# Kernel tuning notes

Hardware: AMD Instinct MI355X
Metric: run time of the kernel (lower is better)

## Reference

```python
import jax, jax.numpy as jnp
import numpy as np

N = 16384      # total ligand atoms
E = 65536      # edges
B = 256        # graphs / batch
MAXN = 64      # atoms per graph (max_nodes for to_dense_batch)
FIN = 64       # num_node_features
HID = 256      # hidden_channels
GH = 2         # gat heads
LP = 1024      # protein length
NH = 4         # cross-attention heads
HD = HID // NH
VOCAB = 22


def setup_inputs() -> dict:
    key = jax.random.key(0)
    ks = jax.random.split(key, 48)
    f = jnp.float32
    def nrm(k, shape, s=0.05):
        return jax.random.normal(k, shape, f) * s
    inp = {}
    inp["x"] = jax.random.normal(ks[0], (N, FIN), f)
    inp["edge_index"] = jax.random.randint(ks[1], (2, E), 0, N)
    inp["batch"] = jnp.arange(N) // MAXN  # sorted, 64 atoms per graph
    inp["protein_seq"] = jax.random.randint(ks[2], (B, LP), 0, VOCAB)
    # GAT layer 1 (FIN -> HID, GH heads, concat=False)
    inp["w1"] = nrm(ks[3], (FIN, GH * HID)); inp["as1"] = nrm(ks[4], (GH, HID)); inp["ad1"] = nrm(ks[5], (GH, HID)); inp["b1"] = jnp.zeros((HID,), f)
    inp["w2"] = nrm(ks[6], (HID, GH * HID)); inp["as2"] = nrm(ks[7], (GH, HID)); inp["ad2"] = nrm(ks[8], (GH, HID)); inp["b2"] = jnp.zeros((HID,), f)
    inp["w3"] = nrm(ks[9], (HID, GH * HID)); inp["as3"] = nrm(ks[10], (GH, HID)); inp["ad3"] = nrm(ks[11], (GH, HID)); inp["b3"] = jnp.zeros((HID,), f)
    # protein embedding + conv1d (OIH layout)
    inp["emb"] = nrm(ks[12], (VOCAB, HID), 0.1)
    inp["conv_w"] = nrm(ks[13], (HID, HID, 3)); inp["conv_b"] = jnp.zeros((HID,), f)
    # cross-attention MHA
    inp["wq"] = nrm(ks[14], (HID, HID)); inp["bq"] = jnp.zeros((HID,), f)
    inp["wk"] = nrm(ks[15], (HID, HID)); inp["bk"] = jnp.zeros((HID,), f)
    inp["wv"] = nrm(ks[16], (HID, HID)); inp["bv"] = jnp.zeros((HID,), f)
    inp["wo"] = nrm(ks[17], (HID, HID)); inp["bo"] = jnp.zeros((HID,), f)
    inp["ln1_g"] = jnp.ones((HID,), f); inp["ln1_b"] = jnp.zeros((HID,), f)
    inp["ffw1"] = nrm(ks[18], (HID, 4 * HID)); inp["ffb1"] = jnp.zeros((4 * HID,), f)
    inp["ffw2"] = nrm(ks[19], (4 * HID, HID)); inp["ffb2"] = jnp.zeros((HID,), f)
    inp["ln2_g"] = jnp.ones((HID,), f); inp["ln2_b"] = jnp.zeros((HID,), f)
    inp["fc1_w"] = nrm(ks[20], (HID, HID)); inp["fc1_b"] = jnp.zeros((HID,), f)
    inp["fc2_w"] = nrm(ks[21], (HID, 1)); inp["fc2_b"] = jnp.zeros((1,), f)
    return inp


def _gat(x, edge_index, W, a_src, a_dst, bias):
    # PyG GATConv, concat=False (mean over heads), add_self_loops=True
    n = x.shape[0]
    h = (x @ W).reshape(n, GH, HID)                      # [N,GH,C]
    loop = jnp.arange(n)
    src = jnp.concatenate([edge_index[0], loop])
    dst = jnp.concatenate([edge_index[1], loop])
    a_s = jnp.einsum('nhc,hc->nh', h, a_src)             # [N,GH]
    a_d = jnp.einsum('nhc,hc->nh', h, a_dst)
    e = jax.nn.leaky_relu(a_s[src] + a_d[dst], 0.2)      # [E+N,GH]
    emax = jax.ops.segment_max(e, dst, num_segments=n)   # each node has a self-loop
    ex = jnp.exp(e - emax[dst])
    den = jax.ops.segment_sum(ex, dst, num_segments=n)
    alpha = ex / den[dst]                                # [E+N,GH]
    msg = h[src] * alpha[:, :, None]
    out = jax.ops.segment_sum(msg, dst, num_segments=n)  # [N,GH,C]
    return out.mean(axis=1) + bias


def _to_dense_batch(x, batch):
    # batch is sorted node->graph ids; counts per graph <= MAXN
    ones = jnp.ones((x.shape[0],), jnp.int32)
    counts = jax.ops.segment_sum(ones, batch, num_segments=B)
    starts = jnp.cumsum(counts) - counts
    pos = jnp.arange(x.shape[0]) - starts[batch]
    dense = jnp.zeros((B, MAXN, x.shape[1]), x.dtype).at[batch, pos].set(x)
    mask = jnp.zeros((B, MAXN), bool).at[batch, pos].set(True)
    return dense, mask


def _layernorm(x, g, b, eps=1e-5):
    mu = x.mean(-1, keepdims=True)
    var = ((x - mu) ** 2).mean(-1, keepdims=True)
    return (x - mu) * jax.lax.rsqrt(var + eps) * g + b


def reference(x, edge_index, batch, protein_seq,
              w1, as1, ad1, b1, w2, as2, ad2, b2, w3, as3, ad3, b3,
              emb, conv_w, conv_b,
              wq, bq, wk, bk, wv, bv, wo, bo,
              ln1_g, ln1_b, ffw1, ffb1, ffw2, ffb2, ln2_g, ln2_b,
              fc1_w, fc1_b, fc2_w, fc2_b):
    # --- ligand GNN (eval mode: dropout = identity) ---
    h = jax.nn.elu(_gat(x, edge_index, w1, as1, ad1, b1))
    h = jax.nn.elu(_gat(h, edge_index, w2, as2, ad2, b2))
    h = jax.nn.elu(_gat(h, edge_index, w3, as3, ad3, b3))
    lig, lig_mask = _to_dense_batch(h, batch)            # [B,MAXN,HID], [B,MAXN]
    # --- protein branch ---
    p = emb[protein_seq]                                 # [B,LP,HID]
    p = p.transpose(0, 2, 1)                             # [B,HID,LP]
    p = jax.lax.conv_general_dilated(p, conv_w, (1,), [(1, 1)],
                                     dimension_numbers=('NCH', 'OIH', 'NCH'))
    p = jax.nn.relu(p + conv_b[None, :, None]).transpose(0, 2, 1)  # [B,LP,HID]
    kpm = protein_seq == 0                               # key padding mask
    # --- cross attention (query=ligand, key/value=protein) ---
    q = (lig @ wq + bq).reshape(B, MAXN, NH, HD)
    k = (p @ wk + bk).reshape(B, LP, NH, HD)
    v = (p @ wv + bv).reshape(B, LP, NH, HD)
    scores = jnp.einsum('bqhd,bkhd->bhqk', q, k) / np.sqrt(HD).astype(np.float32)
    scores = jnp.where(kpm[:, None, None, :], jnp.float32(-1e9), scores)
    attn = jax.nn.softmax(scores, axis=-1)               # [B,NH,MAXN,LP]
    ctx = jnp.einsum('bhqk,bkhd->bqhd', attn, v).reshape(B, MAXN, HID)
    attn_out = ctx @ wo + bo
    y = _layernorm(lig + attn_out, ln1_g, ln1_b)
    ff = jax.nn.gelu(y @ ffw1 + ffb1, approximate=False) @ ffw2 + ffb2
    y = _layernorm(y + ff, ln2_g, ln2_b)
    # --- masked mean pool ---
    m = lig_mask[:, :, None].astype(y.dtype)
    pooled = (y * m).sum(axis=1) / (m.sum(axis=1) + 1e-6)
    out = jax.nn.relu(pooled @ fc1_w + fc1_b)
    return out @ fc2_w + fc2_b                           # [B,1]
```

## Files before the change

kernel.cpp:

```cpp
#include <hip/hip_runtime.h>
#include <hip/hip_bf16.h>
#include <cstdint>
#include <cstddef>

#define NAT 16384
#define NED 65536
#define BGR 256
#define FIN 64
#define HID 256
#define LPN 1024
#define HD 64
#define NTRIP 11638
#define NTAB  11648

typedef __bf16 bf16x8 __attribute__((ext_vector_type(8)));
typedef float floatx4 __attribute__((ext_vector_type(4)));

__device__ __forceinline__ void gl2lds16(const void* g, void* l)
{
    __builtin_amdgcn_global_load_lds(
        (const __attribute__((address_space(1))) unsigned int*)g,
        (__attribute__((address_space(3))) unsigned int*)l, 16, 0, 0);
}

template<int ACT, int OUTBF16, int BIASROW, int HSPLIT, int NCOL>
__global__ __launch_bounds__(512) void gemm_mfma(const __bf16* __restrict__ A,
    const __bf16* __restrict__ Bt, const float* __restrict__ bias,
    void* __restrict__ Cout, int M, int Nn, int K, float escale)
{
    constexpr int NJ = NCOL / 32;
    __shared__ __bf16 As[2][128][32];
    __shared__ __bf16 Bs[2][NCOL][32];
    const int t = threadIdx.x;
    const int m0 = blockIdx.y * 128, n0 = blockIdx.x * NCOL;
    const int w = t >> 6, lane = t & 63;
    const int wm = (w & 3) * 32, wn = (w >> 2) * (NCOL / 2);
    const int quad = lane >> 4, l16 = lane & 15;
    const int r0 = t >> 2, s0 = t & 3, g0 = (s0 ^ (r0 & 3)) * 8;
    const int fso = (quad ^ (l16 & 3)) * 8;
    floatx4 acc[2][NJ] = {};
    for (int k0 = 0; k0 < K; k0 += 64) {
        gl2lds16(A + (size_t)(m0 + r0) * K + k0 + g0,       &As[0][r0][s0 * 8]);
        gl2lds16(A + (size_t)(m0 + r0) * K + k0 + 32 + g0,  &As[1][r0][s0 * 8]);
        if (NCOL == 128 || t < 256) {
            gl2lds16(Bt + (size_t)(n0 + r0) * K + k0 + g0,      &Bs[0][r0][s0 * 8]);
            gl2lds16(Bt + (size_t)(n0 + r0) * K + k0 + 32 + g0, &Bs[1][r0][s0 * 8]);
        }
        __syncthreads();
#pragma unroll
        for (int c = 0; c < 2; c++) {
            bf16x8 af[2], bfr[NJ];
#pragma unroll
            for (int mi = 0; mi < 2; mi++) af[mi]  = *(const bf16x8*)&As[c][wm + mi * 16 + l16][fso];
#pragma unroll
            for (int nj = 0; nj < NJ; nj++) bfr[nj] = *(const bf16x8*)&Bs[c][wn + nj * 16 + l16][fso];
#pragma unroll
            for (int mi = 0; mi < 2; mi++)
#pragma unroll
                for (int nj = 0; nj < NJ; nj++)
                    acc[mi][nj] = __builtin_amdgcn_mfma_f32_16x16x32_bf16(af[mi], bfr[nj], acc[mi][nj], 0, 0, 0);
        }
        __syncthreads();
    }
#pragma unroll
    for (int mi = 0; mi < 2; mi++)
#pragma unroll
        for (int nj = 0; nj < NJ; nj++) {
            int col = n0 + wn + nj * 16 + l16;
#pragma unroll
            for (int r = 0; r < 4; r++) {
                int row = m0 + wm + mi * 16 + quad * 4 + r;
                float bval = bias ? (BIASROW ? bias[row] : bias[col]) : 0.f;
                float v = (acc[mi][nj][r] + bval) * escale;
                if (ACT == 1) v = fmaxf(v, 0.f);
                if (ACT == 2) v = 0.5f * v * (1.f + erff(v * 0.70710678118654752f));
                if (HSPLIT)      ((__bf16*)Cout)[((size_t)(col >> 6) * M + row) * 64 + (col & 63)] = (__bf16)v;
                else if (OUTBF16) ((__bf16*)Cout)[(size_t)row * Nn + col] = (__bf16)v;
                else              ((float*)Cout)[(size_t)row * Nn + col] = v;
            }
        }
}

__global__ __launch_bounds__(512) void gemm_gat(const __bf16* __restrict__ A,
    const __bf16* __restrict__ Bt, const float* __restrict__ as_f,
    const float* __restrict__ ad_f, __bf16* __restrict__ Hg,
    float* __restrict__ part, int K)
{
    __shared__ __bf16 As[2][128][32];
    __shared__ __bf16 Bs[2][128][32];
    const int t = threadIdx.x;
    const int m0 = blockIdx.y * 128, n0 = blockIdx.x * 128;
    const int w = t >> 6, lane = t & 63;
    const int wm = (w & 3) * 32, wn = (w >> 2) * 64;
    const int quad = lane >> 4, l16 = lane & 15;
    const int r0 = t >> 2, s0 = t & 3, g0 = (s0 ^ (r0 & 3)) * 8;
    const int fso = (quad ^ (l16 & 3)) * 8;
    floatx4 acc[2][4] = {};
    for (int k0 = 0; k0 < K; k0 += 64) {
        gl2lds16(A + (size_t)(m0 + r0) * K + k0 + g0,       &As[0][r0][s0 * 8]);
        gl2lds16(A + (size_t)(m0 + r0) * K + k0 + 32 + g0,  &As[1][r0][s0 * 8]);
        gl2lds16(Bt + (size_t)(n0 + r0) * K + k0 + g0,      &Bs[0][r0][s0 * 8]);
        gl2lds16(Bt + (size_t)(n0 + r0) * K + k0 + 32 + g0, &Bs[1][r0][s0 * 8]);
        __syncthreads();
#pragma unroll
        for (int c = 0; c < 2; c++) {
            bf16x8 af[2], bfr[4];
#pragma unroll
            for (int mi = 0; mi < 2; mi++) af[mi]  = *(const bf16x8*)&As[c][wm + mi * 16 + l16][fso];
#pragma unroll
            for (int nj = 0; nj < 4; nj++) bfr[nj] = *(const bf16x8*)&Bs[c][wn + nj * 16 + l16][fso];
#pragma unroll
            for (int mi = 0; mi < 2; mi++)
#pragma unroll
                for (int nj = 0; nj < 4; nj++)
                    acc[mi][nj] = __builtin_amdgcn_mfma_f32_16x16x32_bf16(af[mi], bfr[nj], acc[mi][nj], 0, 0, 0);
        }
        __syncthreads();
    }
    const int slot = blockIdx.x * 2 + (w >> 2);
#pragma unroll
    for (int mi = 0; mi < 2; mi++) {
#pragma unroll
        for (int r = 0; r < 4; r++) {
            float ps = 0.f, pd = 0.f;
#pragma unroll
            for (int nj = 0; nj < 4; nj++) {
                int col = n0 + wn + nj * 16 + l16;
                float v = acc[mi][nj][r];
                ps += v * as_f[col];
                pd += v * ad_f[col];
            }
#pragma unroll
            for (int off = 1; off < 16; off <<= 1) {
                ps += __shfl_xor(ps, off, 64);
                pd += __shfl_xor(pd, off, 64);
            }
            if (l16 == 0) {
                int row = m0 + wm + mi * 16 + quad * 4 + r;
                part[(size_t)(slot * 2 + 0) * NAT + row] = ps;
                part[(size_t)(slot * 2 + 1) * NAT + row] = pd;
            }
        }
    }
#pragma unroll
    for (int mi = 0; mi < 2; mi++)
#pragma unroll
        for (int nj = 0; nj < 4; nj++) {
            int col = n0 + wn + nj * 16 + l16;
#pragma unroll
            for (int r = 0; r < 4; r++) {
                int row = m0 + wm + mi * 16 + quad * 4 + r;
                Hg[(size_t)row * 512 + col] = (__bf16)acc[mi][nj][r];
            }
        }
}

__global__ void fold_k(const float* __restrict__ part, float* __restrict__ a_s,
                       float* __restrict__ a_d)
{
    int n = blockIdx.x * 256 + threadIdx.x;
    float s0 = 0.f, d0 = 0.f, s1 = 0.f, d1 = 0.f;
#pragma unroll
    for (int sl = 0; sl < 4; sl++) {
        s0 += part[(size_t)(sl * 2 + 0) * NAT + n];
        d0 += part[(size_t)(sl * 2 + 1) * NAT + n];
        s1 += part[(size_t)((sl + 4) * 2 + 0) * NAT + n];
        d1 += part[(size_t)((sl + 4) * 2 + 1) * NAT + n];
    }
    a_s[n * 2 + 0] = s0; a_s[n * 2 + 1] = s1;
    a_d[n * 2 + 0] = d0; a_d[n * 2 + 1] = d1;
}

struct Segs {
    const float* src[12];
    __bf16* dst[12];
    int kdim[12];
    int ndim[12];
    int mode[12];
    int start[13];
};

__global__ __launch_bounds__(256) void misc1_k(const int* __restrict__ ei,
    int* __restrict__ deg, const float* __restrict__ emb,
    const float* __restrict__ cw, float* __restrict__ tap,
    const int* __restrict__ seq, unsigned short* __restrict__ tid,
    Segs S, int total)
{
    const int bid = blockIdx.x;
    const int t = threadIdx.x;
    if (bid < 256) {
        int e = bid * 256 + t;
        atomicAdd(&deg[ei[NED + e]], 1);
    } else if (bid < 520) {
        const int b = bid - 256;
        const int dlv = b >> 2, part = b & 3;
        const int dl = dlv / 22, v = dlv % 22;
        const float* er = emb + v * 256 + part * 64;
        const float* wr = cw + (size_t)t * 768 + part * 192 + dl;
        float s = 0.f;
        for (int k = 0; k < 64; k += 4) {
            s += er[k + 0] * wr[k * 3 + 0];
            s += er[k + 1] * wr[k * 3 + 3];
            s += er[k + 2] * wr[k * 3 + 6];
            s += er[k + 3] * wr[k * 3 + 9];
        }
        atomicAdd(&tap[(size_t)dlv * 256 + t], s);
    } else if (bid < 1544) {
        int i = (bid - 520) * 256 + t;
        int b = i >> 10, l = i & 1023;
        const int* sr = seq + b * LPN;
        int t0 = (l > 0) ? sr[l - 1] : -1;
        int t1 = sr[l];
        int t2 = (l < LPN - 1) ? sr[l + 1] : -1;
        int v = (t0 + 1) * 506 + t1 * 23 + (t2 + 1);
        tid[i] = (unsigned short)(v | (t1 == 0 ? 0x8000 : 0));
    } else {
        int i = (bid - 1544) * 256 + t;
        if (i >= total) return;
        int s = 0;
        while (i >= S.start[s + 1]) s++;
        int j = i - S.start[s];
        if (S.mode[s] == 0) {
            S.dst[s][j] = (__bf16)S.src[s][j];
        } else {
            int K = S.kdim[s], N = S.ndim[s];
            int n = j / K, k = j - n * K;
            S.dst[s][j] = (__bf16)S.src[s][(size_t)k * N + n];
        }
    }
}

__global__ __launch_bounds__(256) void misc2_k(const int* __restrict__ deg,
    int* __restrict__ rowptr, const float* __restrict__ tap,
    const float* __restrict__ bias, __bf16* __restrict__ P)
{
    __shared__ int part[256];
    const int t = threadIdx.x;
    if (blockIdx.x == 0) {
        int base = t * 64;
        int s = 0;
#pragma unroll
        for (int i = 0; i < 64; i++) s += deg[base + i];
        part[t] = s;
        __syncthreads();
        for (int off = 1; off < 256; off <<= 1) {
            int v = (t >= off) ? part[t - off] : 0;
            __syncthreads();
            part[t] += v;
            __syncthreads();
        }
        int run = t ? part[t - 1] : 0;
        for (int i = 0; i < 64; i++) { rowptr[base + i] = run; run += deg[base + i]; }
        if (t == 255) rowptr[16384] = run;
    } else {
        const int row = (blockIdx.x - 1) * 8 + (t >> 5);
        const int c = (t & 31) * 8;
        __bf16 o[8];
        if (row < NTRIP) {
            const int a = row / 506, rem = row - a * 506;
            const int t1 = rem / 23, c2 = rem - t1 * 23;
            float acc[8];
#pragma unroll
            for (int j = 0; j < 8; j++) acc[j] = bias[c + j];
            if (a > 0) {
                const float* r = tap + (size_t)(0 * 22 + (a - 1)) * 256 + c;
#pragma unroll
                for (int j = 0; j < 8; j++) acc[j] += r[j];
            }
            {
                const float* r = tap + (size_t)(1 * 22 + t1) * 256 + c;
#pragma unroll
                for (int j = 0; j < 8; j++) acc[j] += r[j];
            }
            if (c2 > 0) {
                const float* r = tap + (size_t)(2 * 22 + (c2 - 1)) * 256 + c;
#pragma unroll
                for (int j = 0; j < 8; j++) acc[j] += r[j];
            }
#pragma unroll
            for (int j = 0; j < 8; j++) o[j] = (__bf16)fmaxf(acc[j], 0.f);
        } else {
#pragma unroll
            for (int j = 0; j < 8; j++) o[j] = (__bf16)0.f;
        }
        *(uint4*)(P + (size_t)row * 256 + c) = *(uint4*)o;
    }
}

__global__ __launch_bounds__(512) void misc3_k(const int* __restrict__ ei,
    int* __restrict__ fill, const int* __restrict__ rowptr,
    int* __restrict__ csrc, int* __restrict__ cdst,
    const __bf16* __restrict__ A, const __bf16* __restrict__ wkT,
    const __bf16* __restrict__ wvT, const float* __restrict__ bk,
    const float* __restrict__ bv, __bf16* __restrict__ Ktab,
    __bf16* __restrict__ Vtab)
{
    __shared__ __bf16 As[2][128][32];
    __shared__ __bf16 Bs[2][128][32];
    const int t = threadIdx.x;
    if (blockIdx.x < 128) {
        int e = blockIdx.x * 512 + t;
        if (e >= NED) return;
        int d = ei[NED + e];
        int pos = rowptr[d] + atomicAdd(&fill[d], 1);
        csrc[pos] = ei[e];
        cdst[pos] = d;
        return;
    }
    const int lb = blockIdx.x - 128;
    const int bx = lb & 3, by = lb >> 2;
    const int z = bx >> 1;
    const int m0 = by * 128, n0 = (bx & 1) * 128;
    const __bf16* Bt = z ? wvT : wkT;
    const float* bias = z ? bv : bk;
    __bf16* Cout = z ? Vtab : Ktab;
    const int w = t >> 6, lane = t & 63;
    const int wm = (w & 3) * 32, wn = (w >> 2) * 64;
    const int quad = lane >> 4, l16 = lane & 15;
    const int r0 = t >> 2, s0 = t & 3, g0 = (s0 ^ (r0 & 3)) * 8;
    const int fso = (quad ^ (l16 & 3)) * 8;
    floatx4 acc[2][4] = {};
    for (int k0 = 0; k0 < 256; k0 += 64) {
        gl2lds16(A + (size_t)(m0 + r0) * 256 + k0 + g0,       &As[0][r0][s0 * 8]);
        gl2lds16(A + (size_t)(m0 + r0) * 256 + k0 + 32 + g0,  &As[1][r0][s0 * 8]);
        gl2lds16(Bt + (size_t)(n0 + r0) * 256 + k0 + g0,      &Bs[0][r0][s0 * 8]);
        gl2lds16(Bt + (size_t)(n0 + r0) * 256 + k0 + 32 + g0, &Bs[1][r0][s0 * 8]);
        __syncthreads();
#pragma unroll
        for (int c = 0; c < 2; c++) {
            bf16x8 af[2], bfr[4];
#pragma unroll
            for (int mi = 0; mi < 2; mi++) af[mi]  = *(const bf16x8*)&As[c][wm + mi * 16 + l16][fso];
#pragma unroll
            for (int nj = 0; nj < 4; nj++) bfr[nj] = *(const bf16x8*)&Bs[c][wn + nj * 16 + l16][fso];
#pragma unroll
            for (int mi = 0; mi < 2; mi++)
#pragma unroll
                for (int nj = 0; nj < 4; nj++)
                    acc[mi][nj] = __builtin_amdgcn_mfma_f32_16x16x32_bf16(af[mi], bfr[nj], acc[mi][nj], 0, 0, 0);
        }
        __syncthreads();
    }
#pragma unroll
    for (int mi = 0; mi < 2; mi++)
#pragma unroll
        for (int nj = 0; nj < 4; nj++) {
            int col = n0 + wn + nj * 16 + l16;
#pragma unroll
            for (int r = 0; r < 4; r++) {
                int row = m0 + wm + mi * 16 + quad * 4 + r;
                float v = acc[mi][nj][r] + bias[col];
                Cout[((size_t)(col >> 6) * NTAB + row) * 64 + (col & 63)] = (__bf16)v;
            }
        }
}

__global__ __launch_bounds__(256) void gat_agg(const int* __restrict__ rowptr,
    const int* __restrict__ csrc, const __bf16* __restrict__ hgb,
    const float* __restrict__ a_s, const float* __restrict__ a_d,
    const float* __restrict__ bias, float* __restrict__ out, __bf16* __restrict__ outb)
{
    const int wave = threadIdx.x >> 6, lane = threadIdx.x & 63;
    const int d = blockIdx.x * 4 + wave;
    const int beg = rowptr[d], end = rowptr[d + 1];
    float2 as2 = *(const float2*)(a_s + d * 2);
    float2 ad2 = *(const float2*)(a_d + d * 2);
    float e0 = as2.x + ad2.x; e0 = (e0 > 0.f) ? e0 : 0.2f * e0;
    float e1 = as2.y + ad2.y; e1 = (e1 > 0.f) ? e1 : 0.2f * e1;
    float m0 = e0, den0 = 1.f, m1 = e1, den1 = 1.f;
    for (int p = beg; p < end; p++) {
        int s = csrc[p];
        float2 av = *(const float2*)(a_s + s * 2);
        float f0 = av.x + ad2.x; f0 = (f0 > 0.f) ? f0 : 0.2f * f0;
        float f1 = av.y + ad2.y; f1 = (f1 > 0.f) ? f1 : 0.2f * f1;
        float nm0 = fmaxf(m0, f0);
        den0 = den0 * __expf(m0 - nm0) + __expf(f0 - nm0);
        m0 = nm0;
        float nm1 = fmaxf(m1, f1);
        den1 = den1 * __expf(m1 - nm1) + __expf(f1 - nm1);
        m1 = nm1;
    }
    const float inv0 = 1.f / den0, inv1 = 1.f / den1;
    const int ch = lane * 8;
    const int g = ch >> 8;
    const float mg = g ? m1 : m0, invg = g ? inv1 : inv0;
    float acc[8] = {};
    {
        float al = __expf((g ? e1 : e0) - mg) * invg;
        bf16x8 hv = *(const bf16x8*)(hgb + (size_t)d * 512 + ch);
#pragma unroll
        for (int j = 0; j < 8; j++) acc[j] += (float)hv[j] * al;
    }
    for (int p = beg; p < end; p++) {
        int s = csrc[p];
        float2 av = *(const float2*)(a_s + s * 2);
        float f0 = av.x + ad2.x; f0 = (f0 > 0.f) ? f0 : 0.2f * f0;
        float f1 = av.y + ad2.y; f1 = (f1 > 0.f) ? f1 : 0.2f * f1;
        float al = __expf((g ? f1 : f0) - mg) * invg;
        bf16x8 hv = *(const bf16x8*)(hgb + (size_t)s * 512 + ch);
#pragma unroll
        for (int j = 0; j < 8; j++) acc[j] += (float)hv[j] * al;
    }
    float other[8];
#pragma unroll
    for (int j = 0; j < 8; j++) other[j] = __shfl_xor(acc[j], 32, 64);
    if (lane < 32) {
#pragma unroll
        for (int j = 0; j < 8; j++) {
            float v = 0.5f * (acc[j] + other[j]) + bias[ch + j];
            v = (v > 0.f) ? v : expm1f(v);
            if (out) out[(size_t)d * 256 + ch + j] = v;
            outb[(size_t)d * 256 + ch + j] = (__bf16)v;
        }
    }
}

__global__ __launch_bounds__(256, 4) void attn6_k(const __bf16* __restrict__ Qb,
    const __bf16* __restrict__ Ktab, const __bf16* __restrict__ Vtab,
    const unsigned short* __restrict__ tid16, __bf16* __restrict__ O)
{
    __shared__ __bf16 Ks[2][4096];
    __shared__ __bf16 Vs[4096];
    __shared__ __bf16 Ps2[4][16][64];
    __shared__ float mask_f[1024];
    __shared__ unsigned short tids[1024];
    const int t = threadIdx.x;
    const int bid = blockIdx.x;
    const int h = (bid >> 1) & 3;
    const int b = ((bid >> 3) << 1) | (bid & 1);
    const int w = t >> 6, lane = t & 63;
    const int quad = lane >> 4, l16 = lane & 15;
    const int key = (l16 & 7) << 4;
    const __bf16* Kh = Ktab + (size_t)h * NTAB * 64;
    const __bf16* Vh = Vtab + (size_t)h * NTAB * 64;
    {
        const uint32_t* src = (const uint32_t*)(tid16 + (size_t)b * LPN);
        uint32_t v0 = src[t], v1 = src[t + 256];
        ((uint32_t*)tids)[t] = v0;
        ((uint32_t*)tids)[t + 256] = v1;
        mask_f[2 * t + 0] = (v0 & 0x8000u) ? -1e9f : 0.f;
        mask_f[2 * t + 1] = (v0 & 0x80000000u) ? -1e9f : 0.f;
        mask_f[2 * (t + 256) + 0] = (v1 & 0x8000u) ? -1e9f : 0.f;
        mask_f[2 * (t + 256) + 1] = (v1 & 0x80000000u) ? -1e9f : 0.f;
    }
    const __bf16* qrow = Qb + (size_t)(b * 64 + w * 16 + l16) * HID + h * HD;
    bf16x8 aq0 = *(const bf16x8*)(qrow + quad * 8);
    bf16x8 aq1 = *(const bf16x8*)(qrow + 32 + quad * 8);
    __syncthreads();

    auto stageK = [&](int kt, int bufb) {
#pragma unroll
        for (int it = 0; it < 2; it++) {
            const int s = it * 256 + t;
            const int pos = s >> 3;
            const int c = (s & 7) ^ (pos & 7);
            const int row = tids[kt * 64 + pos] & 0x7fff;
            gl2lds16(Kh + (size_t)row * 64 + c * 8,
                     &Ks[bufb][(it * 256 + w * 64) * 8]);
        }
    };
    auto loadV = [&](int kt, bf16x8* vrr) {
#pragma unroll
        for (int it = 0; it < 2; it++) {
            const int pos = w * 8 + (lane >> 3) + it * 32;
            const int row = tids[kt * 64 + pos] & 0x7fff;
            vrr[it] = *(const bf16x8*)(Vh + (size_t)row * 64 + (lane & 7) * 8);
        }
    };
    auto writeV = [&](const bf16x8* vrr) {
        const int p = lane >> 3, c = lane & 7;
#pragma unroll
        for (int it = 0; it < 2; it++) {
            const int pos = w * 8 + p + it * 32;
            const int cp = pos >> 3;
#pragma unroll
            for (int j = 0; j < 8; j++) {
                const int chl = c * 8 + j;
                Vs[chl * 64 + (((cp ^ c ^ j) & 7) << 3) + p] = vrr[it][j];
            }
        }
    };

    bf16x8 vr[2];
    stageK(0, 0);
    loadV(0, vr);
    writeV(vr);
    float m_run = -3e38f;
    float l_run = 0.f;
    floatx4 ctx[4] = {};
    __syncthreads();

    for (int kt = 0; kt < 16; kt++) {
        const int buf = kt & 1;
        const int kp0 = kt * 64;
        if (kt < 15) {
            stageK(kt + 1, buf ^ 1);
            loadV(kt + 1, vr);
        }
        const int ksl0 = (quad ^ (l16 & 7)) * 8;
        const int ksl1 = ((quad + 4) ^ (l16 & 7)) * 8;
        floatx4 s[4];
#pragma unroll
        for (int nj = 0; nj < 4; nj++) {
            const __bf16* kr = &Ks[buf][(nj * 16 + l16) * 64];
            bf16x8 k0 = *(const bf16x8*)&kr[ksl0];
            bf16x8 k1 = *(const bf16x8*)&kr[ksl1];
            floatx4 z = {0.f, 0.f, 0.f, 0.f};
            s[nj] = __builtin_amdgcn_mfma_f32_16x16x32_bf16(k0, aq0, z, 0, 0, 0);
            s[nj] = __builtin_amdgcn_mfma_f32_16x16x32_bf16(k1, aq1, s[nj], 0, 0, 0);
        }
#pragma unroll
        for (int nj = 0; nj < 4; nj++) {
            floatx4 m4 = *(const floatx4*)&mask_f[kp0 + nj * 16 + quad * 4];
#pragma unroll
            for (int r = 0; r < 4; r++) s[nj][r] += m4[r];
        }
        float mx = -3e38f;
#pragma unroll
        for (int nj = 0; nj < 4; nj++)
#pragma unroll
            for (int r = 0; r < 4; r++) mx = fmaxf(mx, s[nj][r]);
        mx = fmaxf(mx, __shfl_xor(mx, 16, 64));
        mx = fmaxf(mx, __shfl_xor(mx, 32, 64));
        const float mn = fmaxf(m_run, mx);
        const float alpha = __expf(m_run - mn);
        m_run = mn;
        float rs = 0.f;
#pragma unroll
        for (int nj = 0; nj < 4; nj++)
#pragma unroll
            for (int r = 0; r < 4; r++) {
                float p = __expf(s[nj][r] - mn);
                s[nj][r] = p;
                rs += p;
            }
        rs += __shfl_xor(rs, 16, 64);
        rs += __shfl_xor(rs, 32, 64);
        l_run = l_run * alpha + rs;
        float al[4];
#pragma unroll
        for (int r = 0; r < 4; r++) al[r] = __shfl(alpha, quad * 4 + r, 64);
        {
            char* rowp = (char*)&Ps2[w][l16][0];
#pragma unroll
            for (int nj = 0; nj < 4; nj++) {
                union { uint2 u2; unsigned short us[4]; } pk;
#pragma unroll
                for (int r = 0; r < 4; r++) {
                    __bf16 bv = (__bf16)s[nj][r];
                    pk.us[r] = *(unsigned short*)&bv;
                }
                *(uint2*)(rowp + ((nj * 32 + quad * 8) ^ key)) = pk.u2;
            }
        }
        bf16x8 pa0 = *(const bf16x8*)((char*)&Ps2[w][l16][0] + ((quad * 16) ^ key));
        bf16x8 pa1 = *(const bf16x8*)((char*)&Ps2[w][l16][0] + ((64 + quad * 16) ^ key));
#pragma unroll
        for (int dj = 0; dj < 4; dj++) {
#pragma unroll
            for (int r = 0; r < 4; r++) ctx[dj][r] *= al[r];
            const int chl = dj * 16 + l16;
            const int Xc = ((chl >> 3) ^ (chl & 7)) & 7;
            bf16x8 bv0 = *(const bf16x8*)&Vs[chl * 64 + (((quad ^ Xc) & 7) << 3)];
            bf16x8 bv1 = *(const bf16x8*)&Vs[chl * 64 + ((((quad + 4) ^ Xc) & 7) << 3)];
            ctx[dj] = __builtin_amdgcn_mfma_f32_16x16x32_bf16(pa0, bv0, ctx[dj], 0, 0, 0);
            ctx[dj] = __builtin_amdgcn_mfma_f32_16x16x32_bf16(pa1, bv1, ctx[dj], 0, 0, 0);
        }
        __syncthreads();
        if (kt < 15) writeV(vr);
        __syncthreads();
    }
    float ll[4];
#pragma unroll
    for (int r = 0; r < 4; r++) ll[r] = __shfl(l_run, quad * 4 + r, 64);
#pragma unroll
    for (int dj = 0; dj < 4; dj++)
#pragma unroll
        for (int r = 0; r < 4; r++) {
            int q = w * 16 + quad * 4 + r;
            O[((size_t)(b * 64 + q)) * 256 + h * HD + dj * 16 + l16] = (__bf16)(ctx[dj][r] / ll[r]);
        }
}

__device__ __forceinline__ float blockSum256(float v, float* red)
{
#pragma unroll
    for (int off = 32; off >= 1; off >>= 1) v += __shfl_down(v, off, 64);
    int wave = threadIdx.x >> 6, lane = threadIdx.x & 63;
    if (lane == 0) red[wave] = v;
    __syncthreads();
    float s = red[0] + red[1] + red[2] + red[3];
    __syncthreads();
    return s;
}

__global__ __launch_bounds__(256) void lnres_k(const float* __restrict__ A,
    const float* __restrict__ Bb, const float* __restrict__ g,
    const float* __restrict__ be, float* __restrict__ Y, __bf16* __restrict__ Yb)
{
    __shared__ float red[4];
    int r = blockIdx.x, t = threadIdx.x;
    float v = A[(size_t)r * 256 + t] + Bb[(size_t)r * 256 + t];
    float mean = blockSum256(v, red) * (1.f / 256.f);
    float d = v - mean;
    float var = blockSum256(d * d, red) * (1.f / 256.f);
    float o = d * rsqrtf(var + 1e-5f) * g[t] + be[t];
    Y[(size_t)r * 256 + t] = o;
    if (Yb) Yb[(size_t)r * 256 + t] = (__bf16)o;
}

__global__ __launch_bounds__(256) void head_k(const float* __restrict__ Y,
    const float* __restrict__ fc1w, const float* __restrict__ fc1b,
    const float* __restrict__ fc2w, const float* __restrict__ fc2b,
    float* __restrict__ out)
{
    __shared__ float pooled[256];
    __shared__ float h[256];
    __shared__ float red[4];
    int b = blockIdx.x, t = threadIdx.x;
    float s = 0.f;
#pragma unroll 8
    for (int q = 0; q < 64; q++) s += Y[(size_t)(b * 64 + q) * 256 + t];
    pooled[t] = s / (64.f + 1e-6f);
    __syncthreads();
    float a = 0.f;
    for (int k = 0; k < 256; k += 4) {
        a += pooled[k + 0] * fc1w[(k + 0) * 256 + t];
        a += pooled[k + 1] * fc1w[(k + 1) * 256 + t];
        a += pooled[k + 2] * fc1w[(k + 2) * 256 + t];
        a += pooled[k + 3] * fc1w[(k + 3) * 256 + t];
    }
    h[t] = fmaxf(a + fc1b[t], 0.f);
    __syncthreads();
    float p = h[t] * fc2w[t];
    p = blockSum256(p, red);
    if (t == 0) out[b] = p + fc2b[0];
}

extern "C" void kernel_launch(void* const* d_in, const int* in_sizes, int n_in,
                              void* d_out, int out_size, void* d_ws, size_t ws_size,
                              hipStream_t stream)
{
    const float* x     = (const float*)d_in[0];
    const int*   ei    = (const int*)d_in[1];
    const int*   pseq  = (const int*)d_in[3];
    const float* w1  = (const float*)d_in[4];
    const float* as1 = (const float*)d_in[5];
    const float* ad1 = (const float*)d_in[6];
    const float* b1  = (const float*)d_in[7];
    const float* w2  = (const float*)d_in[8];
    const float* as2 = (const float*)d_in[9];
    const float* ad2 = (const float*)d_in[10];
    const float* b2  = (const float*)d_in[11];
    const float* w3  = (const float*)d_in[12];
    const float* as3 = (const float*)d_in[13];
    const float* ad3 = (const float*)d_in[14];
    const float* b3  = (const float*)d_in[15];
    const float* emb    = (const float*)d_in[16];
    const float* conv_w = (const float*)d_in[17];
    const float* conv_b = (const float*)d_in[18];
    const float* wq = (const float*)d_in[19];
    const float* bq = (const float*)d_in[20];
    const float* wk = (const float*)d_in[21];
    const float* bk = (const float*)d_in[22];
    const float* wv = (const float*)d_in[23];
    const float* bv = (const float*)d_in[24];
    const float* wo = (const float*)d_in[25];
    const float* bo = (const float*)d_in[26];
    const float* ln1_g = (const float*)d_in[27];
    const float* ln1_b = (const float*)d_in[28];
    const float* ffw1  = (const float*)d_in[29];
    const float* ffb1  = (const float*)d_in[30];
    const float* ffw2  = (const float*)d_in[31];
    const float* ffb2  = (const float*)d_in[32];
    const float* ln2_g = (const float*)d_in[33];
    const float* ln2_b = (const float*)d_in[34];
    const float* fc1_w = (const float*)d_in[35];
    const float* fc1_b = (const float*)d_in[36];
    const float* fc2_w = (const float*)d_in[37];
    const float* fc2_b = (const float*)d_in[38];
    (void)in_sizes; (void)n_in; (void)out_size;

    char* ws = (char*)d_ws;
    size_t off = 0;
    auto alloc = [&](size_t bytes) -> char* {
        char* p = ws + off;
        off += (bytes + 255) & ~(size_t)255;
        return p;
    };
    __bf16* hgb  = (__bf16*)alloc((size_t)NAT * 512 * 2);
    float* og    = (float*)alloc((size_t)NAT * 512 * 4);
    float* hb0   = (float*)alloc((size_t)NAT * 256 * 4);
    float* hb1   = (float*)alloc((size_t)NAT * 256 * 4);
    __bf16* xb   = (__bf16*)alloc((size_t)NAT * FIN * 2);
    __bf16* hbb  = (__bf16*)alloc((size_t)NAT * 256 * 2);
    __bf16* qbb  = (__bf16*)alloc((size_t)NAT * 256 * 2);
    __bf16* ctxbb= (__bf16*)alloc((size_t)NAT * 256 * 2);
    __bf16* ybb  = (__bf16*)alloc((size_t)NAT * 256 * 2);
    float* a_s   = (float*)alloc((size_t)NAT * 2 * 4);
    float* a_d   = (float*)alloc((size_t)NAT * 2 * 4);
    float* asd_p = (float*)alloc((size_t)16 * NAT * 4);
    int* deg     = (int*)alloc((size_t)NAT * 4);
    int* fill    = (int*)alloc((size_t)NAT * 4);
    int* rowptr  = (int*)alloc((size_t)(NAT + 1) * 4);
    int* csrc    = (int*)alloc((size_t)NED * 4);
    int* cdst    = (int*)alloc((size_t)NED * 4);
    float* tap   = (float*)alloc((size_t)3 * 22 * 256 * 4);
    __bf16* ptab = (__bf16*)alloc((size_t)NTAB * 256 * 2);
    __bf16* Ktab = (__bf16*)alloc((size_t)NTAB * 256 * 2);
    __bf16* Vtab = (__bf16*)alloc((size_t)NTAB * 256 * 2);
    unsigned short* tid16 = (unsigned short*)alloc((size_t)BGR * LPN * 2);
    __bf16* w1T  = (__bf16*)alloc((size_t)512 * 64 * 2);
    __bf16* w2T  = (__bf16*)alloc((size_t)512 * 256 * 2);
    __bf16* w3T  = (__bf16*)alloc((size_t)512 * 256 * 2);
    __bf16* wkT  = (__bf16*)alloc((size_t)256 * 256 * 2);
    __bf16* wvT  = (__bf16*)alloc((size_t)256 * 256 * 2);
    __bf16* wqT  = (__bf16*)alloc((size_t)256 * 256 * 2);
    __bf16* woT  = (__bf16*)alloc((size_t)256 * 256 * 2);
    __bf16* f1T  = (__bf16*)alloc((size_t)1024 * 256 * 2);
    __bf16* f2T  = (__bf16*)alloc((size_t)256 * 1024 * 2);
    size_t fixed_end = off;
    char* region   = ws + fixed_end;
    __bf16* ffbb   = (__bf16*)region;
    float*  y2     = (float*)(region + (size_t)NAT * 1024 * 2);
    float* attno = og;
    float* ybuf  = og + (size_t)NAT * 256;
    float* ff2o  = hb1;
    (void)ws_size;

    hipMemsetAsync(deg, 0, (size_t)NAT * 8, stream);
    hipMemsetAsync(tap, 0, (size_t)3 * 22 * 256 * 4, stream);

    int cvt_total;
    {
        Segs S;
        const float* srcs[10] = {x, w1, w2, w3, wk, wv, wq, wo, ffw1, ffw2};
        __bf16* dsts[10] = {xb, w1T, w2T, w3T, wkT, wvT, wqT, woT, f1T, f2T};
        int kd[10] = {0, 64, 256, 256, 256, 256, 256, 256, 256, 1024};
        int nd[10] = {0, 512, 512, 512, 256, 256, 256, 256, 1024, 256};
        int md[10] = {0, 1, 1, 1, 1, 1, 1, 1, 1, 1};
        int cnt[10] = {NAT * FIN, 32768, 131072, 131072,
                       65536, 65536, 65536, 65536, 262144, 262144};
        int run = 0;
        for (int i = 0; i < 10; i++) {
            S.src[i] = srcs[i]; S.dst[i] = dsts[i];
            S.kdim[i] = kd[i]; S.ndim[i] = nd[i]; S.mode[i] = md[i];
            S.start[i] = run; run += cnt[i];
        }
        S.start[10] = run; S.start[11] = run; S.start[12] = run;
        cvt_total = run;
        int grid1 = 1544 + (run + 255) / 256;
        misc1_k<<<grid1, 256, 0, stream>>>(ei, deg, emb, conv_w, tap, pseq, tid16, S, run);
    }

    misc2_k<<<1 + NTAB / 8, 256, 0, stream>>>(deg, rowptr, tap, conv_b, ptab);

    misc3_k<<<128 + 4 * (NTAB / 128), 512, 0, stream>>>(ei, fill, rowptr, csrc, cdst,
                                                        ptab, wkT, wvT, bk, bv, Ktab, Vtab);

    const __bf16* WT[3] = {w1T, w2T, w3T};
    const float* asl[3] = {as1, as2, as3};
    const float* adl[3] = {ad1, ad2, ad3};
    const float* bl[3]  = {b1, b2, b3};
    float* houts[3] = {nullptr, nullptr, hb0};
    const __bf16* hinb = xb;
    int Kdim = FIN;
    for (int l = 0; l < 3; l++) {
        gemm_gat<<<dim3(4, NAT / 128), 512, 0, stream>>>(hinb, WT[l], asl[l], adl[l], hgb, asd_p, Kdim);
        fold_k<<<NAT / 256, 256, 0, stream>>>(asd_p, a_s, a_d);
        gat_agg<<<NAT / 4, 256, 0, stream>>>(rowptr, csrc, hgb, a_s, a_d, bl[l], houts[l], hbb);
        hinb = hbb;
        Kdim = HID;
    }
    const float* lig = hb0;
    const __bf16* ligb = hbb;

    gemm_mfma<0, 1, 0, 0, 64><<<dim3(4, NAT / 128), 512, 0, stream>>>(ligb, wqT, bq, qbb, NAT, 256, 256, 0.125f);

    attn6_k<<<BGR * 4, 256, 0, stream>>>(qbb, Ktab, Vtab, tid16, ctxbb);

    gemm_mfma<0, 0, 0, 0, 64><<<dim3(4, NAT / 128), 512, 0, stream>>>(ctxbb, woT, bo, attno, NAT, 256, 256, 1.f);
    lnres_k<<<NAT, 256, 0, stream>>>(lig, attno, ln1_g, ln1_b, ybuf, ybb);
    gemm_mfma<2, 1, 0, 0, 128><<<dim3(8, NAT / 128), 512, 0, stream>>>(ybb, f1T, ffb1, ffbb, NAT, 1024, 256, 1.f);
    gemm_mfma<0, 0, 0, 0, 64><<<dim3(4, NAT / 128), 512, 0, stream>>>(ffbb, f2T, ffb2, ff2o, NAT, 256, 1024, 1.f);
    lnres_k<<<NAT, 256, 0, stream>>>(ybuf, ff2o, ln2_g, ln2_b, y2, nullptr);

    head_k<<<BGR, 256, 0, stream>>>(y2, fc1_w, fc1_b, fc2_w, fc2_b, (float*)d_out);
}
```

Before: 475.0 us.

## Precompute GAT attention projections via W·a and fuse final layernorm into pooling head

Folds the attention vectors into the layer weights (W·a_src, W·a_dst) once, so per-node attention logits come from the layer input instead of a reduction inside the GEMM epilogue. This removes the partial-sum output and the fold kernel. The next layer's logits are now computed inside gat_agg from the freshly produced activations, and layer 1's logits come from extra blocks in misc3. Separately, the second residual layernorm is fused into the pooling head, which drops a full write and read of the output buffer, and the conv tap precompute no longer needs a memset or atomics. Numerics shift slightly because the logits are computed from fp32 activations rather than the bf16-rounded GEMM output.

```diff
diff --git a/kernel.cpp b/kernel.cpp
--- a/kernel.cpp
+++ b/kernel.cpp
@@ -82,9 +82,7 @@
 }
 
 __global__ __launch_bounds__(512) void gemm_gat(const __bf16* __restrict__ A,
-    const __bf16* __restrict__ Bt, const float* __restrict__ as_f,
-    const float* __restrict__ ad_f, __bf16* __restrict__ Hg,
-    float* __restrict__ part, int K)
+    const __bf16* __restrict__ Bt, __bf16* __restrict__ Hg, int K)
 {
     __shared__ __bf16 As[2][128][32];
     __shared__ __bf16 Bs[2][128][32];
@@ -117,31 +115,6 @@
         }
         __syncthreads();
     }
-    const int slot = blockIdx.x * 2 + (w >> 2);
-#pragma unroll
-    for (int mi = 0; mi < 2; mi++) {
-#pragma unroll
-        for (int r = 0; r < 4; r++) {
-            float ps = 0.f, pd = 0.f;
-#pragma unroll
-            for (int nj = 0; nj < 4; nj++) {
-                int col = n0 + wn + nj * 16 + l16;
-                float v = acc[mi][nj][r];
-                ps += v * as_f[col];
-                pd += v * ad_f[col];
-            }
-#pragma unroll
-            for (int off = 1; off < 16; off <<= 1) {
-                ps += __shfl_xor(ps, off, 64);
-                pd += __shfl_xor(pd, off, 64);
-            }
-            if (l16 == 0) {
-                int row = m0 + wm + mi * 16 + quad * 4 + r;
-                part[(size_t)(slot * 2 + 0) * NAT + row] = ps;
-                part[(size_t)(slot * 2 + 1) * NAT + row] = pd;
-            }
-        }
-    }
 #pragma unroll
     for (int mi = 0; mi < 2; mi++)
 #pragma unroll
@@ -153,22 +126,6 @@
                 Hg[(size_t)row * 512 + col] = (__bf16)acc[mi][nj][r];
             }
         }
-}
-
-__global__ void fold_k(const float* __restrict__ part, float* __restrict__ a_s,
-                       float* __restrict__ a_d)
-{
-    int n = blockIdx.x * 256 + threadIdx.x;
-    float s0 = 0.f, d0 = 0.f, s1 = 0.f, d1 = 0.f;
-#pragma unroll
-    for (int sl = 0; sl < 4; sl++) {
-        s0 += part[(size_t)(sl * 2 + 0) * NAT + n];
-        d0 += part[(size_t)(sl * 2 + 1) * NAT + n];
-        s1 += part[(size_t)((sl + 4) * 2 + 0) * NAT + n];
-        d1 += part[(size_t)((sl + 4) * 2 + 1) * NAT + n];
-    }
-    a_s[n * 2 + 0] = s0; a_s[n * 2 + 1] = s1;
-    a_d[n * 2 + 0] = d0; a_d[n * 2 + 1] = d1;
 }
 
 struct Segs {
@@ -184,6 +141,12 @@
     int* __restrict__ deg, const float* __restrict__ emb,
     const float* __restrict__ cw, float* __restrict__ tap,
     const int* __restrict__ seq, unsigned short* __restrict__ tid,
+    const float* __restrict__ wl0, const float* __restrict__ wl1,
+    const float* __restrict__ wl2,
+    const float* __restrict__ as1, const float* __restrict__ as2,
+    const float* __restrict__ as3,
+    const float* __restrict__ ad1, const float* __restrict__ ad2,
+    const float* __restrict__ ad3, float* __restrict__ wasd,
     Segs S, int total)
 {
     const int bid = blockIdx.x;
@@ -191,22 +154,21 @@
     if (bid < 256) {
         int e = bid * 256 + t;
         atomicAdd(&deg[ei[NED + e]], 1);
-    } else if (bid < 520) {
-        const int b = bid - 256;
-        const int dlv = b >> 2, part = b & 3;
+    } else if (bid < 322) {
+        const int dlv = bid - 256;
         const int dl = dlv / 22, v = dlv % 22;
-        const float* er = emb + v * 256 + part * 64;
-        const float* wr = cw + (size_t)t * 768 + part * 192 + dl;
+        const float* er = emb + v * 256;
+        const float* wr = cw + (size_t)t * 768 + dl;
         float s = 0.f;
-        for (int k = 0; k < 64; k += 4) {
-            s += er[k + 0] * wr[k * 3 + 0];
-            s += er[k + 1] * wr[k * 3 + 3];
-            s += er[k + 2] * wr[k * 3 + 6];
-            s += er[k + 3] * wr[k * 3 + 9];
-        }
-        atomicAdd(&tap[(size_t)dlv * 256 + t], s);
-    } else if (bid < 1544) {
-        int i = (bid - 520) * 256 + t;
+        for (int k = 0; k < 256; k += 4) {
+            s += er[k + 0] * wr[(k + 0) * 3];
+            s += er[k + 1] * wr[(k + 1) * 3];
+            s += er[k + 2] * wr[(k + 2) * 3];
+            s += er[k + 3] * wr[(k + 3) * 3];
+        }
+        tap[(size_t)dlv * 256 + t] = s;
+    } else if (bid < 1346) {
+        int i = (bid - 322) * 256 + t;
         int b = i >> 10, l = i & 1023;
         const int* sr = seq + b * LPN;
         int t0 = (l > 0) ? sr[l - 1] : -1;
@@ -214,8 +176,24 @@
         int t2 = (l < LPN - 1) ? sr[l + 1] : -1;
         int v = (t0 + 1) * 506 + t1 * 23 + (t2 + 1);
         tid[i] = (unsigned short)(v | (t1 == 0 ? 0x8000 : 0));
+    } else if (bid < 1349) {
+        const int l = bid - 1346;
+        const int Kl = l ? 256 : 64;
+        if (t < Kl) {
+            const float* Wr = (l == 0 ? wl0 : (l == 1 ? wl1 : wl2)) + (size_t)t * 512;
+            const float* asl = (l == 0 ? as1 : (l == 1 ? as2 : as3));
+            const float* adl = (l == 0 ? ad1 : (l == 1 ? ad2 : ad3));
+            float s0 = 0.f, s1 = 0.f, d0 = 0.f, d1 = 0.f;
+            for (int c = 0; c < 256; c++) {
+                float w0 = Wr[c], w1v = Wr[256 + c];
+                s0 += w0 * asl[c];       s1 += w1v * asl[256 + c];
+                d0 += w0 * adl[c];       d1 += w1v * adl[256 + c];
+            }
+            float* o = wasd + (size_t)(l * 256 + t) * 4;
+            o[0] = s0; o[1] = s1; o[2] = d0; o[3] = d1;
+        }
     } else {
-        int i = (bid - 1544) * 256 + t;
+        int i = (bid - 1349) * 256 + t;
         if (i >= total) return;
         int s = 0;
         while (i >= S.start[s + 1]) s++;
@@ -293,7 +271,9 @@
     const __bf16* __restrict__ A, const __bf16* __restrict__ wkT,
     const __bf16* __restrict__ wvT, const float* __restrict__ bk,
     const float* __restrict__ bv, __bf16* __restrict__ Ktab,
-    __bf16* __restrict__ Vtab)
+    __bf16* __restrict__ Vtab,
+    const __bf16* __restrict__ xb, const float* __restrict__ wasd0,
+    float* __restrict__ as0, float* __restrict__ ad0)
 {
     __shared__ __bf16 As[2][128][32];
     __shared__ __bf16 Bs[2][128][32];
@@ -305,6 +285,30 @@
         int pos = rowptr[d] + atomicAdd(&fill[d], 1);
         csrc[pos] = ei[e];
         cdst[pos] = d;
+        return;
+    }
+    if (blockIdx.x >= 492) {
+        const int node = (blockIdx.x - 492) * 64 + (t >> 3);
+        const int l8 = t & 7;
+        bf16x8 xv = *(const bf16x8*)(xb + (size_t)node * 64 + l8 * 8);
+        float p0 = 0.f, p1 = 0.f, p2 = 0.f, p3 = 0.f;
+#pragma unroll
+        for (int j = 0; j < 8; j++) {
+            float xf = (float)xv[j];
+            float4 w4 = *(const float4*)(wasd0 + (size_t)(l8 * 8 + j) * 4);
+            p0 += xf * w4.x; p1 += xf * w4.y; p2 += xf * w4.z; p3 += xf * w4.w;
+        }
+#pragma unroll
+        for (int off = 1; off < 8; off <<= 1) {
+            p0 += __shfl_xor(p0, off, 64);
+            p1 += __shfl_xor(p1, off, 64);
+            p2 += __shfl_xor(p2, off, 64);
+            p3 += __shfl_xor(p3, off, 64);
+        }
+        if (l8 == 0) {
+            as0[node * 2 + 0] = p0; as0[node * 2 + 1] = p1;
+            ad0[node * 2 + 0] = p2; ad0[node * 2 + 1] = p3;
+        }
         return;
     }
     const int lb = blockIdx.x - 128;
@@ -358,7 +362,9 @@
 __global__ __launch_bounds__(256) void gat_agg(const int* __restrict__ rowptr,
     const int* __restrict__ csrc, const __bf16* __restrict__ hgb,
     const float* __restrict__ a_s, const float* __restrict__ a_d,
-    const float* __restrict__ bias, float* __restrict__ out, __bf16* __restrict__ outb)
+    const float* __restrict__ bias, const float* __restrict__ wasd_next,
+    float* __restrict__ as_out, float* __restrict__ ad_out,
+    float* __restrict__ out, __bf16* __restrict__ outb)
 {
     const int wave = threadIdx.x >> 6, lane = threadIdx.x & 63;
     const int d = blockIdx.x * 4 + wave;
@@ -405,12 +411,34 @@
 #pragma unroll
     for (int j = 0; j < 8; j++) other[j] = __shfl_xor(acc[j], 32, 64);
     if (lane < 32) {
+        float vv[8];
 #pragma unroll
         for (int j = 0; j < 8; j++) {
             float v = 0.5f * (acc[j] + other[j]) + bias[ch + j];
             v = (v > 0.f) ? v : expm1f(v);
+            vv[j] = v;
             if (out) out[(size_t)d * 256 + ch + j] = v;
             outb[(size_t)d * 256 + ch + j] = (__bf16)v;
+        }
+        if (wasd_next) {
+            float p0 = 0.f, p1 = 0.f, p2 = 0.f, p3 = 0.f;
+#pragma unroll
+            for (int j = 0; j < 8; j++) {
+                float4 w4 = *(const float4*)(wasd_next + (size_t)(ch + j) * 4);
+                p0 += vv[j] * w4.x; p1 += vv[j] * w4.y;
+                p2 += vv[j] * w4.z; p3 += vv[j] * w4.w;
+            }
+#pragma unroll
+            for (int off = 1; off < 32; off <<= 1) {
+                p0 += __shfl_xor(p0, off, 64);
+                p1 += __shfl_xor(p1, off, 64);
+                p2 += __shfl_xor(p2, off, 64);
+                p3 += __shfl_xor(p3, off, 64);
+            }
+            if (lane == 0) {
+                as_out[d * 2 + 0] = p0; as_out[d * 2 + 1] = p1;
+                ad_out[d * 2 + 0] = p2; ad_out[d * 2 + 1] = p3;
+            }
         }
     }
 }
@@ -609,19 +637,50 @@
     if (Yb) Yb[(size_t)r * 256 + t] = (__bf16)o;
 }
 
-__global__ __launch_bounds__(256) void head_k(const float* __restrict__ Y,
+__global__ __launch_bounds__(256) void head2_k(const float* __restrict__ A,
+    const float* __restrict__ Bb, const float* __restrict__ g,
+    const float* __restrict__ be,
     const float* __restrict__ fc1w, const float* __restrict__ fc1b,
     const float* __restrict__ fc2w, const float* __restrict__ fc2b,
     float* __restrict__ out)
 {
+    __shared__ float pooled4[4][256];
     __shared__ float pooled[256];
     __shared__ float h[256];
     __shared__ float red[4];
-    int b = blockIdx.x, t = threadIdx.x;
-    float s = 0.f;
-#pragma unroll 8
-    for (int q = 0; q < 64; q++) s += Y[(size_t)(b * 64 + q) * 256 + t];
-    pooled[t] = s / (64.f + 1e-6f);
+    const int b = blockIdx.x, t = threadIdx.x;
+    const int wv = t >> 6, lane = t & 63;
+    const int ch = lane * 4;
+    float g0 = g[ch], g1 = g[ch + 1], g2 = g[ch + 2], g3 = g[ch + 3];
+    float b0 = be[ch], b1v = be[ch + 1], b2v = be[ch + 2], b3v = be[ch + 3];
+    float accp0 = 0.f, accp1 = 0.f, accp2 = 0.f, accp3 = 0.f;
+    for (int r = wv; r < 64; r += 4) {
+        const size_t base = (size_t)(b * 64 + r) * 256 + ch;
+        float v0 = A[base + 0] + Bb[base + 0];
+        float v1 = A[base + 1] + Bb[base + 1];
+        float v2 = A[base + 2] + Bb[base + 2];
+        float v3 = A[base + 3] + Bb[base + 3];
+        float s = v0 + v1 + v2 + v3;
+#pragma unroll
+        for (int off = 32; off >= 1; off >>= 1) s += __shfl_xor(s, off, 64);
+        float mean = s * (1.f / 256.f);
+        float c0 = v0 - mean, c1 = v1 - mean, c2 = v2 - mean, c3 = v3 - mean;
+        float s2 = c0 * c0 + c1 * c1 + c2 * c2 + c3 * c3;
+#pragma unroll
+        for (int off = 32; off >= 1; off >>= 1) s2 += __shfl_xor(s2, off, 64);
+        float rstd = rsqrtf(s2 * (1.f / 256.f) + 1e-5f);
+        accp0 += c0 * rstd * g0 + b0;
+        accp1 += c1 * rstd * g1 + b1v;
+        accp2 += c2 * rstd * g2 + b2v;
+        accp3 += c3 * rstd * g3 + b3v;
+    }
+    pooled4[wv][ch + 0] = accp0;
+    pooled4[wv][ch + 1] = accp1;
+    pooled4[wv][ch + 2] = accp2;
+    pooled4[wv][ch + 3] = accp3;
+    __syncthreads();
+    pooled[t] = (pooled4[0][t] + pooled4[1][t] + pooled4[2][t] + pooled4[3][t])
+                / (64.f + 1e-6f);
     __syncthreads();
     float a = 0.f;
     for (int k = 0; k < 256; k += 4) {
@@ -697,9 +756,11 @@
     __bf16* qbb  = (__bf16*)alloc((size_t)NAT * 256 * 2);
     __bf16* ctxbb= (__bf16*)alloc((size_t)NAT * 256 * 2);
     __bf16* ybb  = (__bf16*)alloc((size_t)NAT * 256 * 2);
-    float* a_s   = (float*)alloc((size_t)NAT * 2 * 4);
-    float* a_d   = (float*)alloc((size_t)NAT * 2 * 4);
-    float* asd_p = (float*)alloc((size_t)16 * NAT * 4);
+    float* asA   = (float*)alloc((size_t)NAT * 2 * 4);
+    float* adA   = (float*)alloc((size_t)NAT * 2 * 4);
+    float* asB   = (float*)alloc((size_t)NAT * 2 * 4);
+    float* adB   = (float*)alloc((size_t)NAT * 2 * 4);
+    float* wasd  = (float*)alloc((size_t)3 * 256 * 4 * 4);
     int* deg     = (int*)alloc((size_t)NAT * 4);
     int* fill    = (int*)alloc((size_t)NAT * 4);
     int* rowptr  = (int*)alloc((size_t)(NAT + 1) * 4);
@@ -722,16 +783,13 @@
     size_t fixed_end = off;
     char* region   = ws + fixed_end;
     __bf16* ffbb   = (__bf16*)region;
-    float*  y2     = (float*)(region + (size_t)NAT * 1024 * 2);
     float* attno = og;
     float* ybuf  = og + (size_t)NAT * 256;
     float* ff2o  = hb1;
     (void)ws_size;
 
     hipMemsetAsync(deg, 0, (size_t)NAT * 8, stream);
-    hipMemsetAsync(tap, 0, (size_t)3 * 22 * 256 * 4, stream);
-
-    int cvt_total;
+
     {
         Segs S;
         const float* srcs[10] = {x, w1, w2, w3, wk, wv, wq, wo, ffw1, ffw2};
@@ -748,27 +806,33 @@
             S.start[i] = run; run += cnt[i];
         }
         S.start[10] = run; S.start[11] = run; S.start[12] = run;
-        cvt_total = run;
-        int grid1 = 1544 + (run + 255) / 256;
-        misc1_k<<<grid1, 256, 0, stream>>>(ei, deg, emb, conv_w, tap, pseq, tid16, S, run);
+        int grid1 = 1349 + (run + 255) / 256;
+        misc1_k<<<grid1, 256, 0, stream>>>(ei, deg, emb, conv_w, tap, pseq, tid16,
+                                           w1, w2, w3, as1, as2, as3, ad1, ad2, ad3,
+                                           wasd, S, run);
     }
 
     misc2_k<<<1 + NTAB / 8, 256, 0, stream>>>(deg, rowptr, tap, conv_b, ptab);
 
-    misc3_k<<<128 + 4 * (NTAB / 128), 512, 0, stream>>>(ei, fill, rowptr, csrc, cdst,
-                                                        ptab, wkT, wvT, bk, bv, Ktab, Vtab);
+    misc3_k<<<128 + 4 * (NTAB / 128) + NAT / 64, 512, 0, stream>>>(
+        ei, fill, rowptr, csrc, cdst, ptab, wkT, wvT, bk, bv, Ktab, Vtab,
+        xb, wasd, asA, adA);
 
     const __bf16* WT[3] = {w1T, w2T, w3T};
-    const float* asl[3] = {as1, as2, as3};
-    const float* adl[3] = {ad1, ad2, ad3};
     const float* bl[3]  = {b1, b2, b3};
     float* houts[3] = {nullptr, nullptr, hb0};
+    const float* asr[3] = {asA, asB, asA};
+    const float* adr[3] = {adA, adB, adA};
+    float* asw[3] = {asB, asA, nullptr};
+    float* adw[3] = {adB, adA, nullptr};
     const __bf16* hinb = xb;
     int Kdim = FIN;
     for (int l = 0; l < 3; l++) {
-        gemm_gat<<<dim3(4, NAT / 128), 512, 0, stream>>>(hinb, WT[l], asl[l], adl[l], hgb, asd_p, Kdim);
-        fold_k<<<NAT / 256, 256, 0, stream>>>(asd_p, a_s, a_d);
-        gat_agg<<<NAT / 4, 256, 0, stream>>>(rowptr, csrc, hgb, a_s, a_d, bl[l], houts[l], hbb);
+        gemm_gat<<<dim3(4, NAT / 128), 512, 0, stream>>>(hinb, WT[l], hgb, Kdim);
+        const float* wnext = (l < 2) ? (wasd + (size_t)(l + 1) * 256 * 4) : nullptr;
+        gat_agg<<<NAT / 4, 256, 0, stream>>>(rowptr, csrc, hgb, asr[l], adr[l],
+                                             bl[l], wnext, asw[l], adw[l],
+                                             houts[l], hbb);
         hinb = hbb;
         Kdim = HID;
     }
@@ -783,7 +847,6 @@
     lnres_k<<<NAT, 256, 0, stream>>>(lig, attno, ln1_g, ln1_b, ybuf, ybb);
     gemm_mfma<2, 1, 0, 0, 128><<<dim3(8, NAT / 128), 512, 0, stream>>>(ybb, f1T, ffb1, ffbb, NAT, 1024, 256, 1.f);
     gemm_mfma<0, 0, 0, 0, 64><<<dim3(4, NAT / 128), 512, 0, stream>>>(ffbb, f2T, ffb2, ff2o, NAT, 256, 1024, 1.f);
-    lnres_k<<<NAT, 256, 0, stream>>>(ybuf, ff2o, ln2_g, ln2_b, y2, nullptr);
-
-    head_k<<<BGR, 256, 0, stream>>>(y2, fc1_w, fc1_b, fc2_w, fc2_b, (float*)d_out);
-}
+    head2_k<<<BGR, 256, 0, stream>>>(ybuf, ff2o, ln2_g, ln2_b,
+                                     fc1_w, fc1_b, fc2_w, fc2_b, (float*)d_out);
+}
```

Result: slower. 485.8 us (+2.3%).
